# Optimization experiments

Hardware: AMD Instinct MI355X
Metric: run time of the kernel (lower is better)

The kernel has to match this reference:

```python
import jax, jax.numpy as jnp
import numpy as np

B, S, HID = 1, 2048, 2048
H, HD, DR = 16, 128, 64
CKV, CQ = 512, 1536
ROPE_BASE = 10000.0


def _rope_cos_sin(seq_len, dim, dtype):
    inv_freq = 1.0 / (ROPE_BASE ** (jnp.arange(0, dim, 2, dtype=jnp.float32) / dim))
    t = jnp.arange(seq_len, dtype=jnp.float32)
    freqs = jnp.outer(t, inv_freq)                      # [S, DR/2]
    emb = jnp.concatenate([freqs, freqs], axis=-1)      # [S, DR]
    return jnp.cos(emb).astype(dtype), jnp.sin(emb).astype(dtype)


def _rotate_half(x):
    x1, x2 = jnp.split(x, 2, axis=-1)
    return jnp.concatenate([-x2, x1], axis=-1)


def _xavier(key, fan_in, fan_out):
    lim = np.sqrt(6.0 / (fan_in + fan_out))
    return jax.random.uniform(key, (fan_in, fan_out), jnp.float32, -lim, lim)


def setup_inputs() -> dict:
    key = jax.random.key(0)
    ks = jax.random.split(key, 10)
    hidden_states = jax.random.normal(ks[0], (B, S, HID), jnp.float32)
    # causal mask: 1.0 where position is masked out (j > i)
    mask = jnp.triu(jnp.ones((S, S), jnp.float32), k=1)[None, None]  # [1,1,S,S]
    return {
        "hidden_states": hidden_states,
        "mask": mask,
        "W_DKV": _xavier(ks[1], HID, CKV),
        "W_UK": _xavier(ks[2], CKV, H * HD),
        "W_UV": _xavier(ks[3], CKV, H * HD),
        "W_DQ": _xavier(ks[4], HID, CQ),
        "W_UQ": _xavier(ks[5], CQ, H * HD),
        "W_QR": _xavier(ks[6], CQ, H * DR),
        "W_KR": _xavier(ks[7], HID, DR),
        "W_O": _xavier(ks[8], H * HD, HID),
    }


def reference(hidden_states, mask, W_DKV, W_UK, W_UV, W_DQ, W_UQ, W_QR, W_KR, W_O):
    b, s, _ = hidden_states.shape
    scale = 1.0 / np.sqrt(HD + DR)

    c_KV = hidden_states @ W_DKV                         # [B,S,CKV]
    k_C = (c_KV @ W_UK).reshape(b, s, H, HD)
    v = (c_KV @ W_UV).reshape(b, s, H, HD)
    c_Q = hidden_states @ W_DQ                           # [B,S,CQ]
    q_C = (c_Q @ W_UQ).reshape(b, s, H, HD)
    q_R = (c_Q @ W_QR).reshape(b, s, H, DR)
    k_R = (hidden_states @ W_KR).reshape(b, s, 1, DR)

    cos, sin = _rope_cos_sin(s, DR, hidden_states.dtype)
    cos = cos[None, :, None, :]                          # [1,S,1,DR]
    sin = sin[None, :, None, :]
    q_R = q_R * cos + _rotate_half(q_R) * sin
    k_R = k_R * cos + _rotate_half(k_R) * sin            # [B,S,1,DR], broadcast over heads

    q = jnp.concatenate([q_C, q_R], axis=-1)             # [B,S,H,HD+DR]
    k = jnp.concatenate([k_C, jnp.broadcast_to(k_R, (b, s, H, DR))], axis=-1)

    # [B,H,Sq,Sk]
    scores = jnp.einsum("bqhd,bkhd->bhqk", q, k) * scale
    if mask is not None:
        scores = scores + mask * -1e9                     # broadcast over heads
    probs = jax.nn.softmax(scores, axis=-1)
    out = jnp.einsum("bhqk,bkhd->bqhd", probs, v).reshape(b, s, H * HD)
    return out @ W_O
```

## Files before the change

kernel.cpp:

```cpp
#include <hip/hip_runtime.h>
#include <hip/hip_bf16.h>
#include <math.h>

typedef __hip_bfloat16 bf16;
typedef short s16x8 __attribute__((ext_vector_type(8)));
typedef unsigned short u16x8 __attribute__((ext_vector_type(8)));
typedef float f32x4 __attribute__((ext_vector_type(4)));

#define S_LEN 2048
#define NHEAD 16
#define HDIM  128
#define DROT  64

__device__ __forceinline__ float bf2f(unsigned short u) {
    union { unsigned int i; float f; } v;
    v.i = ((unsigned int)u) << 16;
    return v.f;
}
__device__ __forceinline__ unsigned short f2bf(float f) {
    union { float f; unsigned int i; } v;
    v.f = f;
    unsigned int r = (v.i + 0x7FFFu + ((v.i >> 16) & 1u)) >> 16;
    return (unsigned short)r;
}

__device__ __forceinline__ void load_lds16(const unsigned short* g, unsigned short* l) {
    __builtin_amdgcn_global_load_lds(
        (const __attribute__((address_space(1))) unsigned short*)g,
        (__attribute__((address_space(3))) unsigned short*)l, 16, 0, 0);
}

__device__ __forceinline__ bool is_bf16(const unsigned int* maskw) {
    return maskw[1] != 0x3F800000u;
}

struct PrepDesc {
    const void* in;
    unsigned short* out;
    int R, C, blk_start, nbx, kind;
};
struct PrepBatch { PrepDesc d[8]; };

__global__ __launch_bounds__(256)
void prep_kernel(PrepBatch b, const unsigned int* __restrict__ maskw) {
    const bool fb = is_bf16(maskw);
    __shared__ unsigned short t[64][80];
    PrepDesc dd = b.d[0];
    #pragma unroll
    for (int p = 1; p < 8; ++p)
        if ((int)blockIdx.x >= b.d[p].blk_start) dd = b.d[p];
    const int local = (int)blockIdx.x - dd.blk_start;
    const int tid = threadIdx.x;

    if (dd.kind == 1) {
        const size_t idx = ((size_t)local * 256 + tid) * 8;
        if (fb) {
            *(u16x8*)(dd.out + idx) = *(const u16x8*)((const unsigned short*)dd.in + idx);
        } else {
            const float* p = (const float*)dd.in + idx;
            float4 f0 = *(const float4*)p;
            float4 f1 = *(const float4*)(p + 4);
            u16x8 u;
            u[0] = f2bf(f0.x); u[1] = f2bf(f0.y); u[2] = f2bf(f0.z); u[3] = f2bf(f0.w);
            u[4] = f2bf(f1.x); u[5] = f2bf(f1.y); u[6] = f2bf(f1.z); u[7] = f2bf(f1.w);
            *(u16x8*)(dd.out + idx) = u;
        }
        return;
    }

    const int by = local / dd.nbx, bx = local - by * dd.nbx;
    const int r0 = by << 6, c0 = bx << 6;
    const int tr = tid >> 3;
    const int tc8 = (tid & 7) << 3;
    #pragma unroll
    for (int p = 0; p < 2; ++p) {
        const int r = tr + p * 32;
        const size_t off = (size_t)(r0 + r) * dd.C + c0 + tc8;
        unsigned short v[8];
        if (fb) {
            u16x8 u = *(const u16x8*)((const unsigned short*)dd.in + off);
            #pragma unroll
            for (int j = 0; j < 8; ++j) v[j] = u[j];
        } else {
            const float* p4 = (const float*)dd.in + off;
            float4 f0 = *(const float4*)p4;
            float4 f1 = *(const float4*)(p4 + 4);
            v[0] = f2bf(f0.x); v[1] = f2bf(f0.y); v[2] = f2bf(f0.z); v[3] = f2bf(f0.w);
            v[4] = f2bf(f1.x); v[5] = f2bf(f1.y); v[6] = f2bf(f1.z); v[7] = f2bf(f1.w);
        }
        #pragma unroll
        for (int j = 0; j < 8; ++j) t[tc8 + j][r] = v[j];
    }
    __syncthreads();
    #pragma unroll
    for (int p = 0; p < 2; ++p) {
        const int c = tr + p * 32;
        u16x8 u = *(const u16x8*)&t[c][tc8];
        *(u16x8*)(dd.out + (size_t)(c0 + c) * dd.R + r0 + tc8) = u;
    }
}

__global__ __launch_bounds__(256)
void transpose_conv(const void* __restrict__ in, unsigned short* __restrict__ out,
                    int R, int C, const unsigned int* __restrict__ maskw) {
    const bool fb = is_bf16(maskw);
    __shared__ unsigned short t[64][80];
    const int r0 = blockIdx.y << 6, c0 = blockIdx.x << 6;
    const int tid = threadIdx.x;
    const int tr = tid >> 3;
    const int tc8 = (tid & 7) << 3;
    #pragma unroll
    for (int p = 0; p < 2; ++p) {
        const int r = tr + p * 32;
        const size_t off = (size_t)(r0 + r) * C + c0 + tc8;
        unsigned short v[8];
        if (fb) {
            u16x8 u = *(const u16x8*)((const unsigned short*)in + off);
            #pragma unroll
            for (int j = 0; j < 8; ++j) v[j] = u[j];
        } else {
            const float* p4 = (const float*)in + off;
            float4 f0 = *(const float4*)p4;
            float4 f1 = *(const float4*)(p4 + 4);
            v[0] = f2bf(f0.x); v[1] = f2bf(f0.y); v[2] = f2bf(f0.z); v[3] = f2bf(f0.w);
            v[4] = f2bf(f1.x); v[5] = f2bf(f1.y); v[6] = f2bf(f1.z); v[7] = f2bf(f1.w);
        }
        #pragma unroll
        for (int j = 0; j < 8; ++j) t[tc8 + j][r] = v[j];
    }
    __syncthreads();
    #pragma unroll
    for (int p = 0; p < 2; ++p) {
        const int c = tr + p * 32;
        u16x8 u = *(const u16x8*)&t[c][tc8];
        *(u16x8*)(out + (size_t)(c0 + c) * R + r0 + tc8) = u;
    }
}

struct GemmDesc {
    const unsigned short* A;
    const unsigned short* Bt;
    void* C;
    int M, N, K;
    int nbx;
    int blk_start;
    int ct;
};
struct GemmBatch { GemmDesc d[4]; };

template <int NP, int CMODE>
__global__ __launch_bounds__(256)
void mfma_gemm2(GemmBatch batch, const unsigned int* __restrict__ maskw) {
    __shared__ __align__(16) unsigned short As[2][128 * 32];
    __shared__ __align__(16) unsigned short Bs[2][64 * 32];

    GemmDesc dd = batch.d[0];
    #pragma unroll
    for (int p = 1; p < NP; ++p)
        if ((int)blockIdx.x >= batch.d[p].blk_start) dd = batch.d[p];
    const int local = (int)blockIdx.x - dd.blk_start;
    const int by = local / dd.nbx;
    const int bx = local - by * dd.nbx;
    const int m0 = by << 7, n0 = bx << 6;
    const int K = dd.K;

    const int tid  = threadIdx.x;
    const int lane = tid & 63;
    const int w    = tid >> 6;
    const int wr = w >> 1, wc = w & 1;
    const int l15 = lane & 15, quad = lane >> 4, q8 = quad << 3;

    int srow[2], scol[2];
    #pragma unroll
    for (int i = 0; i < 2; ++i) {
        const int c = (2 * w + i) * 64 + lane;
        srow[i] = c >> 2;
        scol[i] = (c & 3) << 3;
    }
    const int c2 = w * 64 + lane;
    const int brow = c2 >> 2, bcol = (c2 & 3) << 3;

    f32x4 acc[4][2];
    #pragma unroll
    for (int i = 0; i < 4; ++i)
        #pragma unroll
        for (int j = 0; j < 2; ++j) {
            f32x4 z = {0.f, 0.f, 0.f, 0.f};
            acc[i][j] = z;
        }

    #pragma unroll
    for (int i = 0; i < 2; ++i)
        load_lds16(dd.A + (size_t)(m0 + srow[i]) * K + scol[i],
                   As[0] + (2 * w + i) * 512);
    load_lds16(dd.Bt + (size_t)(n0 + brow) * K + bcol, Bs[0] + w * 512);
    __syncthreads();

    int cur = 0;
    for (int k0 = 0; k0 < K; k0 += 32) {
        if (k0 + 32 < K) {
            #pragma unroll
            for (int i = 0; i < 2; ++i)
                load_lds16(dd.A + (size_t)(m0 + srow[i]) * K + k0 + 32 + scol[i],
                           As[cur ^ 1] + (2 * w + i) * 512);
            load_lds16(dd.Bt + (size_t)(n0 + brow) * K + k0 + 32 + bcol,
                       Bs[cur ^ 1] + w * 512);
        }
        s16x8 af[4], bf[2];
        #pragma unroll
        for (int mt = 0; mt < 4; ++mt)
            af[mt] = *(const s16x8*)&As[cur][(wr * 64 + mt * 16 + l15) * 32 + q8];
        #pragma unroll
        for (int nt = 0; nt < 2; ++nt)
            bf[nt] = *(const s16x8*)&Bs[cur][(wc * 32 + nt * 16 + l15) * 32 + q8];
        #pragma unroll
        for (int nt = 0; nt < 2; ++nt)
            #pragma unroll
            for (int mt = 0; mt < 4; ++mt)
                acc[mt][nt] = __builtin_amdgcn_mfma_f32_16x16x32_bf16(
                    af[mt], bf[nt], acc[mt][nt], 0, 0, 0);
        __syncthreads();
        cur ^= 1;
    }

    bool cbf = true;
    if (CMODE == 2) cbf = is_bf16(maskw);
    const int M = dd.M, N = dd.N;
    #pragma unroll
    for (int mt = 0; mt < 4; ++mt)
        #pragma unroll
        for (int nt = 0; nt < 2; ++nt) {
            f32x4 d = acc[mt][nt];
            const int col  = n0 + wc * 32 + nt * 16 + l15;
            const int rowb = m0 + wr * 64 + mt * 16 + quad * 4;
            if (dd.ct) {
                ushort4 o;
                o.x = f2bf(d[0]); o.y = f2bf(d[1]); o.z = f2bf(d[2]); o.w = f2bf(d[3]);
                *(ushort4*)((unsigned short*)dd.C + (size_t)col * M + rowb) = o;
            } else if (cbf) {
                unsigned short* c = (unsigned short*)dd.C + (size_t)rowb * N + col;
                #pragma unroll
                for (int r = 0; r < 4; ++r) c[(size_t)r * N] = f2bf(d[r]);
            } else {
                float* c = (float*)dd.C + (size_t)rowb * N + col;
                #pragma unroll
                for (int r = 0; r < 4; ++r) c[(size_t)r * N] = d[r];
            }
        }
}

__global__ __launch_bounds__(256)
void rope_all(unsigned short* __restrict__ qR, unsigned short* __restrict__ kRb) {
    int bid = blockIdx.x;
    unsigned short* x;
    int nh, stride;
    if (bid < 4096) { x = qR; nh = 16; stride = 64; }
    else            { x = kRb; nh = 1; stride = 128; bid -= 4096; }
    const int idx = bid * 256 + threadIdx.x;
    const int d = idx & 31;
    const int rest = idx >> 5;
    const int h = rest % nh;
    const int s = rest / nh;
    if (s >= S_LEN) return;
    const float inv = powf(10000.0f, -(float)d * (1.0f / 32.0f));
    const float ang = (float)s * inv;
    float si, co;
    sincosf(ang, &si, &co);
    unsigned short* p = x + ((size_t)s * nh + h) * stride;
    const float x1 = bf2f(p[d]);
    const float x2 = bf2f(p[d + 32]);
    p[d]      = f2bf(x1 * co - x2 * si);
    p[d + 32] = f2bf(x2 * co + x1 * si);
}

__global__ __launch_bounds__(512)
void mfma_attn(const unsigned short* __restrict__ qC,
               const unsigned short* __restrict__ qR,
               const unsigned short* __restrict__ kC,
               const unsigned short* __restrict__ kRb,
               const unsigned short* __restrict__ vT,
               unsigned short* __restrict__ at) {
    __shared__ __align__(16) union {
        struct {
            unsigned short Ks[64][200];
            unsigned short Vs[128][72];
            unsigned short Ps[8][16][40];
        } s;
        struct {
            float O[4][16][132];
            float L[4][16];
        } m;
    } sm;

    const int tid  = threadIdx.x;
    const int lane = tid & 63;
    const int w    = tid >> 6;
    const int qs   = w & 3;
    const int kh   = w >> 2;
    const int l15 = lane & 15, quad = lane >> 4, q8 = quad << 3;

    const int bid  = (int)blockIdx.x;
    const int half = bid >> 8;
    const int idx  = bid & 255;
    const int h    = idx & 15;
    const int qhh  = idx >> 4;
    const int qb   = half ? (31 - qhh) : qhh;
    const int q0   = qb << 6;
    const int qrow0 = q0 + qs * 16;

    s16x8 qf[6];
    {
        const int qrow = qrow0 + l15;
        const unsigned short* qCrow = qC + ((size_t)qrow * NHEAD + h) * HDIM;
        #pragma unroll
        for (int s = 0; s < 4; ++s)
            qf[s] = *(const s16x8*)(qCrow + s * 32 + q8);
        const unsigned short* qRrow = qR + ((size_t)qrow * NHEAD + h) * DROT;
        #pragma unroll
        for (int s = 0; s < 2; ++s)
            qf[4 + s] = *(const s16x8*)(qRrow + s * 32 + q8);
    }

    f32x4 accO[8];
    #pragma unroll
    for (int i = 0; i < 8; ++i) { f32x4 z = {0.f, 0.f, 0.f, 0.f}; accO[i] = z; }
    float slocal[4] = {0.f, 0.f, 0.f, 0.f};

    const float scale = 0.0721687836487032f;
    const int ntiles = (q0 >> 6) + 1;

    const int krow = tid >> 3;
    const int kcb  = (tid & 7) * 24;
    const int vd   = tid >> 2;
    const int vcb  = (tid & 3) << 4;

    u16x8 kreg[3], vreg[2];
    {
        #pragma unroll
        for (int m = 0; m < 3; ++m) {
            const int c = kcb + m * 8;
            const unsigned short* src = (c < 128)
                ? kC + ((size_t)krow * NHEAD + h) * HDIM + c
                : kRb + (size_t)krow * 128 + (c - 128);
            kreg[m] = *(const u16x8*)src;
        }
        const unsigned short* vrow = vT + (size_t)(h * HDIM + vd) * S_LEN;
        #pragma unroll
        for (int m = 0; m < 2; ++m)
            vreg[m] = *(const u16x8*)(vrow + vcb + m * 8);
    }

    for (int t = 0; t < ntiles; ++t) {
        const int key0 = t << 6;
        __syncthreads();
        #pragma unroll
        for (int m = 0; m < 3; ++m)
            *(u16x8*)&sm.s.Ks[krow][kcb + m * 8] = kreg[m];
        #pragma unroll
        for (int m = 0; m < 2; ++m)
            *(u16x8*)&sm.s.Vs[vd][vcb + m * 8] = vreg[m];
        __syncthreads();

        if (t + 1 < ntiles) {
            const int kn = key0 + 64;
            #pragma unroll
            for (int m = 0; m < 3; ++m) {
                const int c = kcb + m * 8;
                const unsigned short* src = (c < 128)
                    ? kC + ((size_t)(kn + krow) * NHEAD + h) * HDIM + c
                    : kRb + (size_t)(kn + krow) * 128 + (c - 128);
                kreg[m] = *(const u16x8*)src;
            }
            const unsigned short* vrow = vT + (size_t)(h * HDIM + vd) * S_LEN + kn;
            #pragma unroll
            for (int m = 0; m < 2; ++m)
                vreg[m] = *(const u16x8*)(vrow + vcb + m * 8);
        }

        const int wk0 = key0 + kh * 32;
        const bool active = wk0 <= qrow0 + 15;
        if (active) {
            f32x4 sA[2];
            #pragma unroll
            for (int nt = 0; nt < 2; ++nt) { f32x4 z = {0.f, 0.f, 0.f, 0.f}; sA[nt] = z; }
            #pragma unroll
            for (int s = 0; s < 6; ++s)
                #pragma unroll
                for (int nt = 0; nt < 2; ++nt) {
                    s16x8 kf = *(const s16x8*)&sm.s.Ks[kh * 32 + nt * 16 + l15][s * 32 + q8];
                    sA[nt] = __builtin_amdgcn_mfma_f32_16x16x32_bf16(qf[s], kf, sA[nt], 0, 0, 0);
                }

            const int rbase = qrow0 + quad * 4;
            const bool diag = (wk0 + 31 > qrow0);
            #pragma unroll
            for (int nt = 0; nt < 2; ++nt) {
                const int col = wk0 + nt * 16 + l15;
                #pragma unroll
                for (int r = 0; r < 4; ++r) {
                    float s = sA[nt][r] * scale;
                    if (diag && (col > rbase + r)) s = -1e30f;
                    const float p = __expf(s);
                    slocal[r] += p;
                    sm.s.Ps[w][quad * 4 + r][nt * 16 + l15] = f2bf(p);
                }
            }

            s16x8 pf = *(const s16x8*)&sm.s.Ps[w][l15][q8];
            #pragma unroll
            for (int dt = 0; dt < 8; ++dt) {
                s16x8 vf = *(const s16x8*)&sm.s.Vs[dt * 16 + l15][kh * 32 + q8];
                accO[dt] = __builtin_amdgcn_mfma_f32_16x16x32_bf16(pf, vf, accO[dt], 0, 0, 0);
            }
        }
    }

    float l_r[4];
    #pragma unroll
    for (int r = 0; r < 4; ++r) {
        float sum = slocal[r];
        #pragma unroll
        for (int off = 1; off < 16; off <<= 1)
            sum += __shfl_xor(sum, off, 64);
        l_r[r] = sum;
    }

    __syncthreads();
    if (kh == 1) {
        #pragma unroll
        for (int dt = 0; dt < 8; ++dt)
            #pragma unroll
            for (int r = 0; r < 4; ++r)
                sm.m.O[qs][quad * 4 + r][dt * 16 + l15] = accO[dt][r];
        if (l15 == 0)
            #pragma unroll
            for (int r = 0; r < 4; ++r)
                sm.m.L[qs][quad * 4 + r] = l_r[r];
    }
    __syncthreads();
    if (kh == 0) {
        float linv[4];
        #pragma unroll
        for (int r = 0; r < 4; ++r)
            linv[r] = 1.f / (l_r[r] + sm.m.L[qs][quad * 4 + r]);
        #pragma unroll
        for (int r = 0; r < 4; ++r) {
            const int row = qrow0 + quad * 4 + r;
            unsigned short* dst = at + (size_t)row * (NHEAD * HDIM) + h * HDIM + l15;
            #pragma unroll
            for (int dt = 0; dt < 8; ++dt) {
                const float o = accO[dt][r]
                              + sm.m.O[qs][quad * 4 + r][dt * 16 + l15];
                dst[dt * 16] = f2bf(o * linv[r]);
            }
        }
    }
}

extern "C" void kernel_launch(void* const* d_in, const int* in_sizes, int n_in,
                              void* d_out, int out_size, void* d_ws, size_t ws_size,
                              hipStream_t stream) {
    (void)in_sizes; (void)n_in; (void)out_size; (void)ws_size;

    const void* hs    = d_in[0];
    const unsigned int* maskw = (const unsigned int*)d_in[1];
    const void* W_DKV = d_in[2];
    const void* W_UK  = d_in[3];
    const void* W_UV  = d_in[4];
    const void* W_DQ  = d_in[5];
    const void* W_UQ  = d_in[6];
    const void* W_QR  = d_in[7];
    const void* W_KR  = d_in[8];
    const void* W_O   = d_in[9];

    const size_t M1 = 1048576;
    unsigned short* ws    = (unsigned short*)d_ws;
    unsigned short* cKV   = ws;
    unsigned short* cQ    = ws + 1 * M1;
    unsigned short* kC    = ws + 4 * M1;
    unsigned short* vT    = ws + 8 * M1;
    unsigned short* DKVt  = ws + 8 * M1;
    unsigned short* DQt   = ws + 9 * M1;
    unsigned short* qC    = ws + 12 * M1;
    unsigned short* hs_bf = ws + 12 * M1;
    unsigned short* qR    = ws + 16 * M1;
    unsigned short* kRb   = ws + 18 * M1;
    unsigned short* KRt   = ws + 18 * M1 + 262144;
    unsigned short* at    = ws + 18 * M1 + 524288;
    unsigned short* UKt   = at;
    unsigned short* UVt   = at + 1 * M1;
    unsigned short* QRt   = at + 2 * M1;
    unsigned short* UQt   = ws + 22 * M1 + 524288;
    unsigned short* WOt   = ws;

    const dim3 blk(256);

    {
        PrepBatch b{};
        b.d[0] = { hs,    hs_bf, 0, 0,           0,  0, 1 };
        b.d[1] = { W_DKV, DKVt,  2048,  512,  2048,  8, 0 };
        b.d[2] = { W_DQ,  DQt,   2048, 1536,  2304, 24, 0 };
        b.d[3] = { W_KR,  KRt,   2048,   64,  3072,  1, 0 };
        b.d[4] = { W_UK,  UKt,    512, 2048,  3104, 32, 0 };
        b.d[5] = { W_UV,  UVt,    512, 2048,  3360, 32, 0 };
        b.d[6] = { W_UQ,  UQt,   1536, 2048,  3616, 32, 0 };
        b.d[7] = { W_QR,  QRt,   1536, 1024,  4384, 16, 0 };
        prep_kernel<<<4768, blk, 0, stream>>>(b, maskw);
    }

    {
        GemmBatch b{};
        b.d[0] = { hs_bf, DQt,  (void*)cQ,  2048, 1536, 2048, 24,   0, 0 };
        b.d[1] = { hs_bf, DKVt, (void*)cKV, 2048,  512, 2048,  8, 384, 0 };
        b.d[2] = { hs_bf, KRt,  (void*)kRb, 2048,  128, 2048,  2, 512, 0 };
        b.d[3] = b.d[2];
        mfma_gemm2<3, 1><<<544, blk, 0, stream>>>(b, maskw);
    }

    {
        GemmBatch b{};
        b.d[0] = { cQ,  UQt, (void*)qC, 2048, 2048, 1536, 32,    0, 0 };
        b.d[1] = { cQ,  QRt, (void*)qR, 2048, 1024, 1536, 16,  512, 0 };
        b.d[2] = { cKV, UKt, (void*)kC, 2048, 2048,  512, 32,  768, 0 };
        b.d[3] = { cKV, UVt, (void*)vT, 2048, 2048,  512, 32, 1280, 1 };
        mfma_gemm2<4, 1><<<1792, blk, 0, stream>>>(b, maskw);
    }

    rope_all<<<4352, blk, 0, stream>>>(qR, kRb);

    transpose_conv<<<dim3(32, 32), blk, 0, stream>>>(W_O, WOt, 2048, 2048, maskw);

    mfma_attn<<<512, dim3(512), 0, stream>>>(qC, qR, kC, kRb, vT, at);

    {
        GemmBatch b{};
        b.d[0] = { at, WOt, d_out, 2048, 2048, 2048, 32, 0, 0 };
        b.d[1] = b.d[0]; b.d[2] = b.d[0]; b.d[3] = b.d[0];
        mfma_gemm2<1, 2><<<512, blk, 0, stream>>>(b, maskw);
    }
}
```

Measured before the change: 326.7 us.

## Double GEMM K-tile to 64 and pair causal query blocks per attention block

The GEMM kernel now stages 64-wide K slices (two 32-wide sub-slabs) per iteration, halving loop iterations and barriers at the cost of doubled LDS use. Separately, each attention block now processes two query tiles (qb and 31-qb) sequentially, so every block does equal causal work and only 256 blocks launch. This reduces barrier and loop overhead and evens out load per block, but lowers the number of concurrent attention blocks and may reduce GEMM occupancy.

```diff
diff --git a/kernel.cpp b/kernel.cpp
--- a/kernel.cpp
+++ b/kernel.cpp
@@ -151,8 +151,8 @@
 template <int NP, int CMODE>
 __global__ __launch_bounds__(256)
 void mfma_gemm2(GemmBatch batch, const unsigned int* __restrict__ maskw) {
-    __shared__ __align__(16) unsigned short As[2][128 * 32];
-    __shared__ __align__(16) unsigned short Bs[2][64 * 32];
+    __shared__ __align__(16) unsigned short As[2][128 * 64];
+    __shared__ __align__(16) unsigned short Bs[2][64 * 64];
 
     GemmDesc dd = batch.d[0];
     #pragma unroll
@@ -170,15 +170,24 @@
     const int wr = w >> 1, wc = w & 1;
     const int l15 = lane & 15, quad = lane >> 4, q8 = quad << 3;
 
-    int srow[2], scol[2];
+    int arow[4], acol[4], adst[4];
+    #pragma unroll
+    for (int i = 0; i < 4; ++i) {
+        const int c = 4 * w + i;
+        const int sl = c >> 3, sub = c & 7;
+        arow[i] = sub * 16 + (lane >> 2);
+        acol[i] = sl * 32 + (lane & 3) * 8;
+        adst[i] = sl * 4096 + sub * 512 + lane * 8;
+    }
+    int brow[2], bcol[2], bdst[2];
     #pragma unroll
     for (int i = 0; i < 2; ++i) {
-        const int c = (2 * w + i) * 64 + lane;
-        srow[i] = c >> 2;
-        scol[i] = (c & 3) << 3;
-    }
-    const int c2 = w * 64 + lane;
-    const int brow = c2 >> 2, bcol = (c2 & 3) << 3;
+        const int c = 2 * w + i;
+        const int sl = c >> 2, sub = c & 3;
+        brow[i] = sub * 16 + (lane >> 2);
+        bcol[i] = sl * 32 + (lane & 3) * 8;
+        bdst[i] = sl * 2048 + sub * 512 + lane * 8;
+    }
 
     f32x4 acc[4][2];
     #pragma unroll
@@ -190,35 +199,44 @@
         }
 
     #pragma unroll
+    for (int i = 0; i < 4; ++i)
+        load_lds16(dd.A + (size_t)(m0 + arow[i]) * K + acol[i], As[0] + adst[i]);
+    #pragma unroll
     for (int i = 0; i < 2; ++i)
-        load_lds16(dd.A + (size_t)(m0 + srow[i]) * K + scol[i],
-                   As[0] + (2 * w + i) * 512);
-    load_lds16(dd.Bt + (size_t)(n0 + brow) * K + bcol, Bs[0] + w * 512);
+        load_lds16(dd.Bt + (size_t)(n0 + brow[i]) * K + bcol[i], Bs[0] + bdst[i]);
     __syncthreads();
 
     int cur = 0;
-    for (int k0 = 0; k0 < K; k0 += 32) {
-        if (k0 + 32 < K) {
+    for (int k0 = 0; k0 < K; k0 += 64) {
+        if (k0 + 64 < K) {
+            #pragma unroll
+            for (int i = 0; i < 4; ++i)
+                load_lds16(dd.A + (size_t)(m0 + arow[i]) * K + k0 + 64 + acol[i],
+                           As[cur ^ 1] + adst[i]);
             #pragma unroll
             for (int i = 0; i < 2; ++i)
-                load_lds16(dd.A + (size_t)(m0 + srow[i]) * K + k0 + 32 + scol[i],
-                           As[cur ^ 1] + (2 * w + i) * 512);
-            load_lds16(dd.Bt + (size_t)(n0 + brow) * K + k0 + 32 + bcol,
-                       Bs[cur ^ 1] + w * 512);
-        }
-        s16x8 af[4], bf[2];
+                load_lds16(dd.Bt + (size_t)(n0 + brow[i]) * K + k0 + 64 + bcol[i],
+                           Bs[cur ^ 1] + bdst[i]);
+        }
+        s16x8 af[4][2], bf[2][2];
         #pragma unroll
         for (int mt = 0; mt < 4; ++mt)
-            af[mt] = *(const s16x8*)&As[cur][(wr * 64 + mt * 16 + l15) * 32 + q8];
+            #pragma unroll
+            for (int ks = 0; ks < 2; ++ks)
+                af[mt][ks] = *(const s16x8*)&As[cur][ks * 4096 + (wr * 64 + mt * 16 + l15) * 32 + q8];
         #pragma unroll
         for (int nt = 0; nt < 2; ++nt)
-            bf[nt] = *(const s16x8*)&Bs[cur][(wc * 32 + nt * 16 + l15) * 32 + q8];
-        #pragma unroll
-        for (int nt = 0; nt < 2; ++nt)
-            #pragma unroll
-            for (int mt = 0; mt < 4; ++mt)
-                acc[mt][nt] = __builtin_amdgcn_mfma_f32_16x16x32_bf16(
-                    af[mt], bf[nt], acc[mt][nt], 0, 0, 0);
+            #pragma unroll
+            for (int ks = 0; ks < 2; ++ks)
+                bf[nt][ks] = *(const s16x8*)&Bs[cur][ks * 2048 + (wc * 32 + nt * 16 + l15) * 32 + q8];
+        #pragma unroll
+        for (int ks = 0; ks < 2; ++ks)
+            #pragma unroll
+            for (int nt = 0; nt < 2; ++nt)
+                #pragma unroll
+                for (int mt = 0; mt < 4; ++mt)
+                    acc[mt][nt] = __builtin_amdgcn_mfma_f32_16x16x32_bf16(
+                        af[mt][ks], bf[nt][ks], acc[mt][nt], 0, 0, 0);
         __syncthreads();
         cur ^= 1;
     }
@@ -299,159 +317,162 @@
     const int kh   = w >> 2;
     const int l15 = lane & 15, quad = lane >> 4, q8 = quad << 3;
 
-    const int bid  = (int)blockIdx.x;
-    const int half = bid >> 8;
-    const int idx  = bid & 255;
-    const int h    = idx & 15;
-    const int qhh  = idx >> 4;
-    const int qb   = half ? (31 - qhh) : qhh;
-    const int q0   = qb << 6;
-    const int qrow0 = q0 + qs * 16;
-
-    s16x8 qf[6];
-    {
-        const int qrow = qrow0 + l15;
-        const unsigned short* qCrow = qC + ((size_t)qrow * NHEAD + h) * HDIM;
-        #pragma unroll
-        for (int s = 0; s < 4; ++s)
-            qf[s] = *(const s16x8*)(qCrow + s * 32 + q8);
-        const unsigned short* qRrow = qR + ((size_t)qrow * NHEAD + h) * DROT;
-        #pragma unroll
-        for (int s = 0; s < 2; ++s)
-            qf[4 + s] = *(const s16x8*)(qRrow + s * 32 + q8);
-    }
-
-    f32x4 accO[8];
-    #pragma unroll
-    for (int i = 0; i < 8; ++i) { f32x4 z = {0.f, 0.f, 0.f, 0.f}; accO[i] = z; }
-    float slocal[4] = {0.f, 0.f, 0.f, 0.f};
+    const int bid   = (int)blockIdx.x;
+    const int h     = bid & 15;
+    const int qbase = bid >> 4;
 
     const float scale = 0.0721687836487032f;
-    const int ntiles = (q0 >> 6) + 1;
 
     const int krow = tid >> 3;
     const int kcb  = (tid & 7) * 24;
     const int vd   = tid >> 2;
     const int vcb  = (tid & 3) << 4;
 
-    u16x8 kreg[3], vreg[2];
-    {
-        #pragma unroll
-        for (int m = 0; m < 3; ++m) {
-            const int c = kcb + m * 8;
-            const unsigned short* src = (c < 128)
-                ? kC + ((size_t)krow * NHEAD + h) * HDIM + c
-                : kRb + (size_t)krow * 128 + (c - 128);
-            kreg[m] = *(const u16x8*)src;
-        }
-        const unsigned short* vrow = vT + (size_t)(h * HDIM + vd) * S_LEN;
-        #pragma unroll
-        for (int m = 0; m < 2; ++m)
-            vreg[m] = *(const u16x8*)(vrow + vcb + m * 8);
-    }
-
-    for (int t = 0; t < ntiles; ++t) {
-        const int key0 = t << 6;
-        __syncthreads();
-        #pragma unroll
-        for (int m = 0; m < 3; ++m)
-            *(u16x8*)&sm.s.Ks[krow][kcb + m * 8] = kreg[m];
-        #pragma unroll
-        for (int m = 0; m < 2; ++m)
-            *(u16x8*)&sm.s.Vs[vd][vcb + m * 8] = vreg[m];
-        __syncthreads();
-
-        if (t + 1 < ntiles) {
-            const int kn = key0 + 64;
+    #pragma unroll
+    for (int part = 0; part < 2; ++part) {
+        const int qb = part ? (31 - qbase) : qbase;
+        const int q0 = qb << 6;
+        const int qrow0 = q0 + qs * 16;
+
+        s16x8 qf[6];
+        {
+            const int qrow = qrow0 + l15;
+            const unsigned short* qCrow = qC + ((size_t)qrow * NHEAD + h) * HDIM;
+            #pragma unroll
+            for (int s = 0; s < 4; ++s)
+                qf[s] = *(const s16x8*)(qCrow + s * 32 + q8);
+            const unsigned short* qRrow = qR + ((size_t)qrow * NHEAD + h) * DROT;
+            #pragma unroll
+            for (int s = 0; s < 2; ++s)
+                qf[4 + s] = *(const s16x8*)(qRrow + s * 32 + q8);
+        }
+
+        f32x4 accO[8];
+        #pragma unroll
+        for (int i = 0; i < 8; ++i) { f32x4 z = {0.f, 0.f, 0.f, 0.f}; accO[i] = z; }
+        float slocal[4] = {0.f, 0.f, 0.f, 0.f};
+
+        const int ntiles = (q0 >> 6) + 1;
+
+        u16x8 kreg[3], vreg[2];
+        {
             #pragma unroll
             for (int m = 0; m < 3; ++m) {
                 const int c = kcb + m * 8;
                 const unsigned short* src = (c < 128)
-                    ? kC + ((size_t)(kn + krow) * NHEAD + h) * HDIM + c
-                    : kRb + (size_t)(kn + krow) * 128 + (c - 128);
+                    ? kC + ((size_t)krow * NHEAD + h) * HDIM + c
+                    : kRb + (size_t)krow * 128 + (c - 128);
                 kreg[m] = *(const u16x8*)src;
             }
-            const unsigned short* vrow = vT + (size_t)(h * HDIM + vd) * S_LEN + kn;
+            const unsigned short* vrow = vT + (size_t)(h * HDIM + vd) * S_LEN;
             #pragma unroll
             for (int m = 0; m < 2; ++m)
                 vreg[m] = *(const u16x8*)(vrow + vcb + m * 8);
         }
 
-        const int wk0 = key0 + kh * 32;
-        const bool active = wk0 <= qrow0 + 15;
-        if (active) {
-            f32x4 sA[2];
-            #pragma unroll
-            for (int nt = 0; nt < 2; ++nt) { f32x4 z = {0.f, 0.f, 0.f, 0.f}; sA[nt] = z; }
-            #pragma unroll
-            for (int s = 0; s < 6; ++s)
+        for (int t = 0; t < ntiles; ++t) {
+            const int key0 = t << 6;
+            __syncthreads();
+            #pragma unroll
+            for (int m = 0; m < 3; ++m)
+                *(u16x8*)&sm.s.Ks[krow][kcb + m * 8] = kreg[m];
+            #pragma unroll
+            for (int m = 0; m < 2; ++m)
+                *(u16x8*)&sm.s.Vs[vd][vcb + m * 8] = vreg[m];
+            __syncthreads();
+
+            if (t + 1 < ntiles) {
+                const int kn = key0 + 64;
+                #pragma unroll
+                for (int m = 0; m < 3; ++m) {
+                    const int c = kcb + m * 8;
+                    const unsigned short* src = (c < 128)
+                        ? kC + ((size_t)(kn + krow) * NHEAD + h) * HDIM + c
+                        : kRb + (size_t)(kn + krow) * 128 + (c - 128);
+                    kreg[m] = *(const u16x8*)src;
+                }
+                const unsigned short* vrow = vT + (size_t)(h * HDIM + vd) * S_LEN + kn;
+                #pragma unroll
+                for (int m = 0; m < 2; ++m)
+                    vreg[m] = *(const u16x8*)(vrow + vcb + m * 8);
+            }
+
+            const int wk0 = key0 + kh * 32;
+            const bool active = wk0 <= qrow0 + 15;
+            if (active) {
+                f32x4 sA[2];
+                #pragma unroll
+                for (int nt = 0; nt < 2; ++nt) { f32x4 z = {0.f, 0.f, 0.f, 0.f}; sA[nt] = z; }
+                #pragma unroll
+                for (int s = 0; s < 6; ++s)
+                    #pragma unroll
+                    for (int nt = 0; nt < 2; ++nt) {
+                        s16x8 kf = *(const s16x8*)&sm.s.Ks[kh * 32 + nt * 16 + l15][s * 32 + q8];
+                        sA[nt] = __builtin_amdgcn_mfma_f32_16x16x32_bf16(qf[s], kf, sA[nt], 0, 0, 0);
+                    }
+
+                const int rbase = qrow0 + quad * 4;
+                const bool diag = (wk0 + 31 > qrow0);
                 #pragma unroll
                 for (int nt = 0; nt < 2; ++nt) {
-                    s16x8 kf = *(const s16x8*)&sm.s.Ks[kh * 32 + nt * 16 + l15][s * 32 + q8];
-                    sA[nt] = __builtin_amdgcn_mfma_f32_16x16x32_bf16(qf[s], kf, sA[nt], 0, 0, 0);
+                    const int col = wk0 + nt * 16 + l15;
+                    #pragma unroll
+                    for (int r = 0; r < 4; ++r) {
+                        float s = sA[nt][r] * scale;
+                        if (diag && (col > rbase + r)) s = -1e30f;
+                        const float p = __expf(s);
+                        slocal[r] += p;
+                        sm.s.Ps[w][quad * 4 + r][nt * 16 + l15] = f2bf(p);
+                    }
                 }
 
-            const int rbase = qrow0 + quad * 4;
-            const bool diag = (wk0 + 31 > qrow0);
-            #pragma unroll
-            for (int nt = 0; nt < 2; ++nt) {
-                const int col = wk0 + nt * 16 + l15;
-                #pragma unroll
-                for (int r = 0; r < 4; ++r) {
-                    float s = sA[nt][r] * scale;
-                    if (diag && (col > rbase + r)) s = -1e30f;
-                    const float p = __expf(s);
-                    slocal[r] += p;
-                    sm.s.Ps[w][quad * 4 + r][nt * 16 + l15] = f2bf(p);
+                s16x8 pf = *(const s16x8*)&sm.s.Ps[w][l15][q8];
+                #pragma unroll
+                for (int dt = 0; dt < 8; ++dt) {
+                    s16x8 vf = *(const s16x8*)&sm.s.Vs[dt * 16 + l15][kh * 32 + q8];
+                    accO[dt] = __builtin_amdgcn_mfma_f32_16x16x32_bf16(pf, vf, accO[dt], 0, 0, 0);
                 }
             }
-
-            s16x8 pf = *(const s16x8*)&sm.s.Ps[w][l15][q8];
-            #pragma unroll
-            for (int dt = 0; dt < 8; ++dt) {
-                s16x8 vf = *(const s16x8*)&sm.s.Vs[dt * 16 + l15][kh * 32 + q8];
-                accO[dt] = __builtin_amdgcn_mfma_f32_16x16x32_bf16(pf, vf, accO[dt], 0, 0, 0);
-            }
-        }
-    }
-
-    float l_r[4];
-    #pragma unroll
-    for (int r = 0; r < 4; ++r) {
-        float sum = slocal[r];
-        #pragma unroll
-        for (int off = 1; off < 16; off <<= 1)
-            sum += __shfl_xor(sum, off, 64);
-        l_r[r] = sum;
-    }
-
-    __syncthreads();
-    if (kh == 1) {
-        #pragma unroll
-        for (int dt = 0; dt < 8; ++dt)
+        }
+
+        float l_r[4];
+        #pragma unroll
+        for (int r = 0; r < 4; ++r) {
+            float sum = slocal[r];
+            #pragma unroll
+            for (int off = 1; off < 16; off <<= 1)
+                sum += __shfl_xor(sum, off, 64);
+            l_r[r] = sum;
+        }
+
+        __syncthreads();
+        if (kh == 1) {
+            #pragma unroll
+            for (int dt = 0; dt < 8; ++dt)
+                #pragma unroll
+                for (int r = 0; r < 4; ++r)
+                    sm.m.O[qs][quad * 4 + r][dt * 16 + l15] = accO[dt][r];
+            if (l15 == 0)
+                #pragma unroll
+                for (int r = 0; r < 4; ++r)
+                    sm.m.L[qs][quad * 4 + r] = l_r[r];
+        }
+        __syncthreads();
+        if (kh == 0) {
+            float linv[4];
             #pragma unroll
             for (int r = 0; r < 4; ++r)
-                sm.m.O[qs][quad * 4 + r][dt * 16 + l15] = accO[dt][r];
-        if (l15 == 0)
-            #pragma unroll
-            for (int r = 0; r < 4; ++r)
-                sm.m.L[qs][quad * 4 + r] = l_r[r];
-    }
-    __syncthreads();
-    if (kh == 0) {
-        float linv[4];
-        #pragma unroll
-        for (int r = 0; r < 4; ++r)
-            linv[r] = 1.f / (l_r[r] + sm.m.L[qs][quad * 4 + r]);
-        #pragma unroll
-        for (int r = 0; r < 4; ++r) {
-            const int row = qrow0 + quad * 4 + r;
-            unsigned short* dst = at + (size_t)row * (NHEAD * HDIM) + h * HDIM + l15;
-            #pragma unroll
-            for (int dt = 0; dt < 8; ++dt) {
-                const float o = accO[dt][r]
-                              + sm.m.O[qs][quad * 4 + r][dt * 16 + l15];
-                dst[dt * 16] = f2bf(o * linv[r]);
+                linv[r] = 1.f / (l_r[r] + sm.m.L[qs][quad * 4 + r]);
+            #pragma unroll
+            for (int r = 0; r < 4; ++r) {
+                const int row = qrow0 + quad * 4 + r;
+                unsigned short* dst = at + (size_t)row * (NHEAD * HDIM) + h * HDIM + l15;
+                #pragma unroll
+                for (int dt = 0; dt < 8; ++dt) {
+                    const float o = accO[dt][r]
+                                  + sm.m.O[qs][quad * 4 + r][dt * 16 + l15];
+                    dst[dt * 16] = f2bf(o * linv[r]);
+                }
             }
         }
     }
@@ -530,7 +551,7 @@
 
     transpose_conv<<<dim3(32, 32), blk, 0, stream>>>(W_O, WOt, 2048, 2048, maskw);
 
-    mfma_attn<<<512, dim3(512), 0, stream>>>(qC, qR, kC, kRb, vT, at);
+    mfma_attn<<<256, dim3(512), 0, stream>>>(qC, qR, kC, kRb, vT, at);
 
     {
         GemmBatch b{};
```

After: 305.2 us. -6.6%, faster.
